# Performance work log

Measured on AMD Instinct MI355X. Metric: run time of the kernel, lower is better.

Reference implementation:

```python
import jax, jax.numpy as jnp
import numpy as np

SCALING = 16.0 / 16  # lora_alpha / rank
INIT_THRESHOLD = 0.01


def setup_inputs() -> dict:
    key = jax.random.key(0)
    k1, k2, k3, k4, k5 = jax.random.split(key, 5)
    B, S, D, R = 4, 2048, 4096, 16
    x = jax.random.normal(k1, (B, S, D), dtype=jnp.float32)
    weight = jax.random.normal(k2, (D, D), dtype=jnp.float32) * (1.0 / np.sqrt(D))
    lora_A = jax.random.normal(k3, (R, D), dtype=jnp.float32) * 0.01
    lora_B = jax.random.normal(k4, (D, R), dtype=jnp.float32) * 0.02
    lora_sigma = jax.random.normal(k5, (R,), dtype=jnp.float32)
    return {"x": x, "weight": weight, "lora_A": lora_A, "lora_B": lora_B,
            "lora_sigma": lora_sigma}


def reference(x, weight, lora_A, lora_B, lora_sigma):
    # mask out singular values below threshold, scale B columns
    mask = (jnp.abs(lora_sigma) >= INIT_THRESHOLD).astype(lora_sigma.dtype)
    sigma_masked = lora_sigma * mask                     # [R]
    # delta = (B * sigma) @ A, scaled; materialized as in original module
    delta = (lora_B * sigma_masked[None, :]) @ lora_A    # [out, in]
    delta = delta * SCALING
    base_out = jnp.einsum('bsd,od->bso', x, weight)      # F.linear(x, W)
    lora_out = jnp.einsum('bsd,od->bso', x, delta)       # dropout p=0 -> identity
    return base_out + lora_out
```

## Files before the change

### kernel.cpp

```cpp
#include <hip/hip_runtime.h>

#define D_DIM 4096
#define R_DIM 16
#define SCALING_F 1.0f
#define THRESH 0.01f

typedef __attribute__((ext_vector_type(8))) short short8;
typedef __attribute__((ext_vector_type(4))) float floatx4;

__device__ __forceinline__ unsigned int f2bf(float f) {
  union { float f; unsigned int u; } v; v.f = f;
  unsigned int u = v.u;
  u += 0x7FFFu + ((u >> 16) & 1u);
  return u >> 16;
}

__global__ __launch_bounds__(256) void convert_x_kernel(
    const float* __restrict__ x, unsigned int* __restrict__ xb, int n8) {
  int idx = blockIdx.x * 256 + threadIdx.x;
  if (idx >= n8) return;
  const float4* xp = (const float4*)x;
  float4 v0 = xp[2 * idx];
  float4 v1 = xp[2 * idx + 1];
  uint4 o;
  o.x = f2bf(v0.x) | (f2bf(v0.y) << 16);
  o.y = f2bf(v0.z) | (f2bf(v0.w) << 16);
  o.z = f2bf(v1.x) | (f2bf(v1.y) << 16);
  o.w = f2bf(v1.z) | (f2bf(v1.w) << 16);
  ((uint4*)xb)[idx] = o;
}

__global__ __launch_bounds__(256) void build_weff_kernel(
    const float* __restrict__ W, const float* __restrict__ lA,
    const float* __restrict__ lB, const float* __restrict__ sigma,
    unsigned int* __restrict__ wb) {
  __shared__ float Bs[R_DIM];
  int idx = blockIdx.x * 256 + threadIdx.x;
  int o  = idx >> 10;
  int dq = idx & 1023;
  if (threadIdx.x < R_DIM) {
    float s = sigma[threadIdx.x];
    s = (fabsf(s) >= THRESH) ? s : 0.0f;
    Bs[threadIdx.x] = lB[o * R_DIM + threadIdx.x] * s * SCALING_F;
  }
  __syncthreads();
  float4 acc = ((const float4*)W)[idx];
#pragma unroll
  for (int r = 0; r < R_DIM; ++r) {
    float b = Bs[r];
    float4 a = ((const float4*)(lA + (size_t)r * D_DIM))[dq];
    acc.x += b * a.x; acc.y += b * a.y; acc.z += b * a.z; acc.w += b * a.w;
  }
  uint2 p;
  p.x = f2bf(acc.x) | (f2bf(acc.y) << 16);
  p.y = f2bf(acc.z) | (f2bf(acc.w) << 16);
  ((uint2*)wb)[idx] = p;
}


__device__ __forceinline__ void stage16(const void* g, void* l) {
  __builtin_amdgcn_global_load_lds(
      (const __attribute__((address_space(1))) void*)g,
      (__attribute__((address_space(3))) void*)l, 16, 0, 0);
}

#define LOADA(BUF, QM)                                                         \
  _Pragma("unroll") for (int t = 0; t < 4; ++t) {                              \
    af[t][0] = *(const short8*)(aRd0 + (BUF)*32768 + (QM)*16384 + t*2048);     \
    af[t][1] = *(const short8*)(aRd1 + (BUF)*32768 + (QM)*16384 + t*2048);     \
  }

#define LOADB(BUF, QN)                                                         \
  _Pragma("unroll") for (int j = 0; j < 2; ++j) {                              \
    bf[j][0] = *(const short8*)(bRd0 + (BUF)*32768 + (QN)*16384 + j*2048);     \
    bf[j][1] = *(const short8*)(bRd1 + (BUF)*32768 + (QN)*16384 + j*2048);     \
  }

#define MFMAQ(QM, QN)                                                          \
  _Pragma("unroll") for (int t = 0; t < 4; ++t)                                \
  _Pragma("unroll") for (int j = 0; j < 2; ++j)                                \
    acc[QM][QN][t][j] = __builtin_amdgcn_mfma_f32_16x16x32_bf16(               \
        af[t][0], bf[j][0], acc[QM][QN][t][j], 0, 0, 0);                       \
  _Pragma("unroll") for (int t = 0; t < 4; ++t)                                \
  _Pragma("unroll") for (int j = 0; j < 2; ++j)                                \
    acc[QM][QN][t][j] = __builtin_amdgcn_mfma_f32_16x16x32_bf16(               \
        af[t][1], bf[j][1], acc[QM][QN][t][j], 0, 0, 0);

#define SYNC_MID()                                      \
  __builtin_amdgcn_sched_barrier(0);                    \
  __builtin_amdgcn_s_barrier();                         \
  asm volatile("s_waitcnt lgkmcnt(0)" ::: "memory");    \
  __builtin_amdgcn_sched_barrier(0);                    \
  __builtin_amdgcn_s_setprio(1)

#define SYNC_END()                                      \
  __builtin_amdgcn_s_setprio(0);                        \
  __builtin_amdgcn_sched_barrier(0);                    \
  __builtin_amdgcn_s_barrier();                         \
  __builtin_amdgcn_sched_barrier(0)

#define SYNC_END_VM()                                   \
  __builtin_amdgcn_s_setprio(0);                        \
  __builtin_amdgcn_sched_barrier(0);                    \
  asm volatile("s_waitcnt vmcnt(4)" ::: "memory");      \
  __builtin_amdgcn_s_barrier();                         \
  __builtin_amdgcn_sched_barrier(0)

__global__ __launch_bounds__(512, 2) void gemm_bt_kernel(
    const unsigned short* __restrict__ A,
    const unsigned short* __restrict__ B,
    float* __restrict__ C, int M) {
  __shared__ __align__(16) char lds[131072];

  const int tid  = threadIdx.x;
  const int lane = tid & 63;
  const int wave = tid >> 6;
  const int wm   = wave >> 2;
  const int wn   = wave & 3;
  const int lrow = lane & 15;
  const int lq   = lane >> 4;
  const int r7   = lrow & 7;

  const int bid = blockIdx.x;
  const int cpx = gridDim.x >> 3;
  const int swz = (bid & 7) * cpx + (bid >> 3);
  const int m0 = (swz >> 4) << 8;
  const int n0 = (swz & 15) << 8;

  const int rr8  = tid >> 3;
  const int kgsw = (tid & 7) ^ (rr8 & 7);
  const char* aSrc = (const char*)A + ((size_t)(m0 + rr8) << 13) + (kgsw << 4);
  const int nrow = (rr8 & 31) | ((rr8 & 32) << 1);
  const char* bSrc = (const char*)B + ((size_t)(n0 + nrow) << 13) + (kgsw << 4);
  char* ldsW = lds + wave * 1024;

  const char* aRd0 = lds + wm * 8192 + lrow * 128 + ((lq ^ r7) << 4);
  const char* aRd1 = lds + wm * 8192 + lrow * 128 + (((4 | lq) ^ r7) << 4);
  const char* bRd0 = lds + 65536 + wn * 4096 + lrow * 128 + ((lq ^ r7) << 4);
  const char* bRd1 = lds + 65536 + wn * 4096 + lrow * 128 + (((4 | lq) ^ r7) << 4);

  short8 af[4][2], bf[2][2];
  floatx4 acc[2][2][4][2] = {};

  stage16(aSrc,                     ldsW + 0);
  stage16(aSrc + (128 << 13),       ldsW + 8192);
  stage16(aSrc + (64 << 13),        ldsW + 16384);
  stage16(aSrc + (192 << 13),       ldsW + 24576);
  stage16(bSrc,                     ldsW + 65536);
  stage16(bSrc + (128 << 13),       ldsW + 73728);
  stage16(bSrc + (32 << 13),        ldsW + 81920);
  stage16(bSrc + (160 << 13),       ldsW + 90112);
  stage16(aSrc + 128,               ldsW + 32768);
  stage16(aSrc + (128 << 13) + 128, ldsW + 40960);
  stage16(bSrc + (32 << 13) + 128,  ldsW + 114688);
  stage16(bSrc + (160 << 13) + 128, ldsW + 122880);
  asm volatile("s_waitcnt vmcnt(4)" ::: "memory");
  __builtin_amdgcn_s_barrier();
  __builtin_amdgcn_sched_barrier(0);

  int kb = 0;
#pragma unroll 1
  for (int f = 0; f < 32; ++f) {
    const int k1 = (kb + 128) & 8191;
    const int k2 = (kb + 256) & 8191;
    const int k3 = (kb + 384) & 8191;

    LOADA(0, 0) LOADB(0, 0)
    stage16(aSrc + (64 << 13) + k1,  ldsW + 49152);
    stage16(aSrc + (192 << 13) + k1, ldsW + 57344);
    SYNC_MID();
    MFMAQ(0, 0)
    SYNC_END();

    LOADB(0, 1)
    stage16(bSrc + k1,               ldsW + 98304);
    stage16(bSrc + (128 << 13) + k1, ldsW + 106496);
    SYNC_MID();
    MFMAQ(0, 1)
    SYNC_END();

    LOADA(0, 1)
    stage16(aSrc + k2,               ldsW + 0);
    stage16(aSrc + (128 << 13) + k2, ldsW + 8192);
    SYNC_MID();
    MFMAQ(1, 1)
    SYNC_END();

    LOADB(0, 0)
    stage16(bSrc + (32 << 13) + k2,  ldsW + 81920);
    stage16(bSrc + (160 << 13) + k2, ldsW + 90112);
    SYNC_MID();
    MFMAQ(1, 0)
    SYNC_END_VM();

    LOADA(1, 0) LOADB(1, 0)
    stage16(aSrc + (64 << 13) + k2,  ldsW + 16384);
    stage16(aSrc + (192 << 13) + k2, ldsW + 24576);
    SYNC_MID();
    MFMAQ(0, 0)
    SYNC_END();

    LOADB(1, 1)
    stage16(bSrc + k2,               ldsW + 65536);
    stage16(bSrc + (128 << 13) + k2, ldsW + 73728);
    SYNC_MID();
    MFMAQ(0, 1)
    SYNC_END();

    LOADA(1, 1)
    stage16(aSrc + k3,               ldsW + 32768);
    stage16(aSrc + (128 << 13) + k3, ldsW + 40960);
    SYNC_MID();
    MFMAQ(1, 1)
    SYNC_END();

    LOADB(1, 0)
    stage16(bSrc + (32 << 13) + k3,  ldsW + 114688);
    stage16(bSrc + (160 << 13) + k3, ldsW + 122880);
    SYNC_MID();
    MFMAQ(1, 0)
    SYNC_END_VM();

    kb += 256;
  }

#pragma unroll
  for (int qm = 0; qm < 2; ++qm)
#pragma unroll
    for (int t = 0; t < 4; ++t)
#pragma unroll
      for (int rr = 0; rr < 4; ++rr) {
        float* cp = C +
            (size_t)(m0 + wm * 128 + qm * 64 + t * 16 + lq * 4 + rr) * D_DIM +
            n0 + wn * 64 + lrow;
#pragma unroll
        for (int qn = 0; qn < 2; ++qn)
#pragma unroll
          for (int j = 0; j < 2; ++j)
            cp[qn * 32 + j * 16] = acc[qm][qn][t][j][rr];
      }
}

extern "C" void kernel_launch(void* const* d_in, const int* in_sizes, int n_in,
                              void* d_out, int out_size, void* d_ws, size_t ws_size,
                              hipStream_t stream) {
  const float* x     = (const float*)d_in[0];
  const float* W     = (const float*)d_in[1];
  const float* lA    = (const float*)d_in[2];
  const float* lB    = (const float*)d_in[3];
  const float* sigma = (const float*)d_in[4];
  float* out = (float*)d_out;

  const int M = in_sizes[0] / D_DIM;
  unsigned int* xb = (unsigned int*)d_ws;
  unsigned int* wb = (unsigned int*)((char*)d_ws + (size_t)M * D_DIM * 2);

  const int n8 = in_sizes[0] / 8;
  convert_x_kernel<<<(n8 + 255) / 256, 256, 0, stream>>>(x, xb, n8);

  const int wquads = (D_DIM * D_DIM) / 4;
  build_weff_kernel<<<wquads / 256, 256, 0, stream>>>(W, lA, lB, sigma, wb);

  const int nblocks = (M / 256) * (D_DIM / 256);
  gemm_bt_kernel<<<nblocks, 512, 0, stream>>>(
      (const unsigned short*)xb, (const unsigned short*)wb, out, M);
}
```

Measured before the change: 524.5 us.

## Software-pipeline LDS fragment loads across MFMA phases and merge prep kernels

Restructures the GEMM main loop so LDS-to-register fragment loads for the next phase are issued before the current phase's MFMAs. It uses double-buffered A/B register fragments and partial lgkmcnt waits, with one barrier per phase in place of two. The staging order and vmcnt depth change to keep eight global-to-LDS loads in flight. Separately, the x-conversion and weight-build kernels are fused into a single launch. The aim is to hide LDS latency and barrier overhead, at the cost of more registers and more delicate hazard ordering across the shared LDS buffers.

```diff
diff --git a/kernel.cpp b/kernel.cpp
--- a/kernel.cpp
+++ b/kernel.cpp
@@ -15,46 +15,48 @@
   return u >> 16;
 }
 
-__global__ __launch_bounds__(256) void convert_x_kernel(
-    const float* __restrict__ x, unsigned int* __restrict__ xb, int n8) {
-  int idx = blockIdx.x * 256 + threadIdx.x;
-  if (idx >= n8) return;
-  const float4* xp = (const float4*)x;
-  float4 v0 = xp[2 * idx];
-  float4 v1 = xp[2 * idx + 1];
-  uint4 o;
-  o.x = f2bf(v0.x) | (f2bf(v0.y) << 16);
-  o.y = f2bf(v0.z) | (f2bf(v0.w) << 16);
-  o.z = f2bf(v1.x) | (f2bf(v1.y) << 16);
-  o.w = f2bf(v1.z) | (f2bf(v1.w) << 16);
-  ((uint4*)xb)[idx] = o;
-}
-
-__global__ __launch_bounds__(256) void build_weff_kernel(
+__global__ __launch_bounds__(256) void prep_kernel(
+    const float* __restrict__ x, unsigned int* __restrict__ xb, int n8,
+    int nxblocks,
     const float* __restrict__ W, const float* __restrict__ lA,
     const float* __restrict__ lB, const float* __restrict__ sigma,
     unsigned int* __restrict__ wb) {
   __shared__ float Bs[R_DIM];
-  int idx = blockIdx.x * 256 + threadIdx.x;
-  int o  = idx >> 10;
-  int dq = idx & 1023;
-  if (threadIdx.x < R_DIM) {
-    float s = sigma[threadIdx.x];
-    s = (fabsf(s) >= THRESH) ? s : 0.0f;
-    Bs[threadIdx.x] = lB[o * R_DIM + threadIdx.x] * s * SCALING_F;
-  }
-  __syncthreads();
-  float4 acc = ((const float4*)W)[idx];
-#pragma unroll
-  for (int r = 0; r < R_DIM; ++r) {
-    float b = Bs[r];
-    float4 a = ((const float4*)(lA + (size_t)r * D_DIM))[dq];
-    acc.x += b * a.x; acc.y += b * a.y; acc.z += b * a.z; acc.w += b * a.w;
-  }
-  uint2 p;
-  p.x = f2bf(acc.x) | (f2bf(acc.y) << 16);
-  p.y = f2bf(acc.z) | (f2bf(acc.w) << 16);
-  ((uint2*)wb)[idx] = p;
+  int b = blockIdx.x;
+  if (b < nxblocks) {
+    int idx = b * 256 + threadIdx.x;
+    if (idx >= n8) return;
+    const float4* xp = (const float4*)x;
+    float4 v0 = xp[2 * idx];
+    float4 v1 = xp[2 * idx + 1];
+    uint4 o;
+    o.x = f2bf(v0.x) | (f2bf(v0.y) << 16);
+    o.y = f2bf(v0.z) | (f2bf(v0.w) << 16);
+    o.z = f2bf(v1.x) | (f2bf(v1.y) << 16);
+    o.w = f2bf(v1.z) | (f2bf(v1.w) << 16);
+    ((uint4*)xb)[idx] = o;
+  } else {
+    int idx = (b - nxblocks) * 256 + threadIdx.x;
+    int o  = idx >> 10;
+    int dq = idx & 1023;
+    if (threadIdx.x < R_DIM) {
+      float s = sigma[threadIdx.x];
+      s = (fabsf(s) >= THRESH) ? s : 0.0f;
+      Bs[threadIdx.x] = lB[o * R_DIM + threadIdx.x] * s * SCALING_F;
+    }
+    __syncthreads();
+    float4 acc = ((const float4*)W)[idx];
+#pragma unroll
+    for (int r = 0; r < R_DIM; ++r) {
+      float bb = Bs[r];
+      float4 a = ((const float4*)(lA + (size_t)r * D_DIM))[dq];
+      acc.x += bb * a.x; acc.y += bb * a.y; acc.z += bb * a.z; acc.w += bb * a.w;
+    }
+    uint2 p;
+    p.x = f2bf(acc.x) | (f2bf(acc.y) << 16);
+    p.y = f2bf(acc.z) | (f2bf(acc.w) << 16);
+    ((uint2*)wb)[idx] = p;
+  }
 }
 
 
@@ -64,47 +66,42 @@
       (__attribute__((address_space(3))) void*)l, 16, 0, 0);
 }
 
-#define LOADA(BUF, QM)                                                         \
+#define FENCE() __builtin_amdgcn_sched_barrier(0)
+
+#define WAIT_VM8_BAR()                                  \
+  FENCE();                                              \
+  asm volatile("s_waitcnt vmcnt(8)" ::: "memory");      \
+  __builtin_amdgcn_s_barrier();                         \
+  FENCE()
+
+#define WAIT_LGKM(N)                                    \
+  asm volatile("s_waitcnt lgkmcnt(" #N ")" ::: "memory"); \
+  FENCE()
+
+#define LOADA_TO(DST, BUF, QM)                                                 \
   _Pragma("unroll") for (int t = 0; t < 4; ++t) {                              \
-    af[t][0] = *(const short8*)(aRd0 + (BUF)*32768 + (QM)*16384 + t*2048);     \
-    af[t][1] = *(const short8*)(aRd1 + (BUF)*32768 + (QM)*16384 + t*2048);     \
-  }
-
-#define LOADB(BUF, QN)                                                         \
+    DST[t][0] = *(const short8*)(aRd0 + (BUF)*32768 + (QM)*16384 + t*2048);    \
+    DST[t][1] = *(const short8*)(aRd1 + (BUF)*32768 + (QM)*16384 + t*2048);    \
+  }
+
+#define LOADB_TO(DST, BUF, QN)                                                 \
   _Pragma("unroll") for (int j = 0; j < 2; ++j) {                              \
-    bf[j][0] = *(const short8*)(bRd0 + (BUF)*32768 + (QN)*16384 + j*2048);     \
-    bf[j][1] = *(const short8*)(bRd1 + (BUF)*32768 + (QN)*16384 + j*2048);     \
-  }
-
-#define MFMAQ(QM, QN)                                                          \
+    DST[j][0] = *(const short8*)(bRd0 + (BUF)*32768 + (QN)*16384 + j*2048);    \
+    DST[j][1] = *(const short8*)(bRd1 + (BUF)*32768 + (QN)*16384 + j*2048);    \
+  }
+
+#define MFMA16(QM, QN, AF, BF)                                                 \
+  __builtin_amdgcn_s_setprio(1);                                               \
   _Pragma("unroll") for (int t = 0; t < 4; ++t)                                \
   _Pragma("unroll") for (int j = 0; j < 2; ++j)                                \
     acc[QM][QN][t][j] = __builtin_amdgcn_mfma_f32_16x16x32_bf16(               \
-        af[t][0], bf[j][0], acc[QM][QN][t][j], 0, 0, 0);                       \
+        AF[t][0], BF[j][0], acc[QM][QN][t][j], 0, 0, 0);                       \
   _Pragma("unroll") for (int t = 0; t < 4; ++t)                                \
   _Pragma("unroll") for (int j = 0; j < 2; ++j)                                \
     acc[QM][QN][t][j] = __builtin_amdgcn_mfma_f32_16x16x32_bf16(               \
-        af[t][1], bf[j][1], acc[QM][QN][t][j], 0, 0, 0);
-
-#define SYNC_MID()                                      \
-  __builtin_amdgcn_sched_barrier(0);                    \
-  __builtin_amdgcn_s_barrier();                         \
-  asm volatile("s_waitcnt lgkmcnt(0)" ::: "memory");    \
-  __builtin_amdgcn_sched_barrier(0);                    \
-  __builtin_amdgcn_s_setprio(1)
-
-#define SYNC_END()                                      \
-  __builtin_amdgcn_s_setprio(0);                        \
-  __builtin_amdgcn_sched_barrier(0);                    \
-  __builtin_amdgcn_s_barrier();                         \
-  __builtin_amdgcn_sched_barrier(0)
-
-#define SYNC_END_VM()                                   \
-  __builtin_amdgcn_s_setprio(0);                        \
-  __builtin_amdgcn_sched_barrier(0);                    \
-  asm volatile("s_waitcnt vmcnt(4)" ::: "memory");      \
-  __builtin_amdgcn_s_barrier();                         \
-  __builtin_amdgcn_sched_barrier(0)
+        AF[t][1], BF[j][1], acc[QM][QN][t][j], 0, 0, 0);                       \
+  __builtin_amdgcn_s_setprio(0);                                               \
+  FENCE()
 
 __global__ __launch_bounds__(512, 2) void gemm_bt_kernel(
     const unsigned short* __restrict__ A,
@@ -139,24 +136,30 @@
   const char* bRd0 = lds + 65536 + wn * 4096 + lrow * 128 + ((lq ^ r7) << 4);
   const char* bRd1 = lds + 65536 + wn * 4096 + lrow * 128 + (((4 | lq) ^ r7) << 4);
 
-  short8 af[4][2], bf[2][2];
+  short8 afX[4][2], afY[4][2];
+  short8 bf0A[2][2], bf0B[2][2];
+  short8 bf1[2][2];
   floatx4 acc[2][2][4][2] = {};
 
-  stage16(aSrc,                     ldsW + 0);
-  stage16(aSrc + (128 << 13),       ldsW + 8192);
-  stage16(aSrc + (64 << 13),        ldsW + 16384);
-  stage16(aSrc + (192 << 13),       ldsW + 24576);
-  stage16(bSrc,                     ldsW + 65536);
-  stage16(bSrc + (128 << 13),       ldsW + 73728);
-  stage16(bSrc + (32 << 13),        ldsW + 81920);
-  stage16(bSrc + (160 << 13),       ldsW + 90112);
-  stage16(aSrc + 128,               ldsW + 32768);
-  stage16(aSrc + (128 << 13) + 128, ldsW + 40960);
-  stage16(bSrc + (32 << 13) + 128,  ldsW + 114688);
-  stage16(bSrc + (160 << 13) + 128, ldsW + 122880);
-  asm volatile("s_waitcnt vmcnt(4)" ::: "memory");
+  stage16(aSrc,                      ldsW + 0);
+  stage16(aSrc + (128 << 13),        ldsW + 8192);
+  stage16(bSrc,                      ldsW + 65536);
+  stage16(bSrc + (128 << 13),        ldsW + 73728);
+  stage16(bSrc + (32 << 13),         ldsW + 81920);
+  stage16(bSrc + (160 << 13),        ldsW + 90112);
+  stage16(aSrc + (64 << 13),         ldsW + 16384);
+  stage16(aSrc + (192 << 13),        ldsW + 24576);
+  stage16(aSrc + 128,                ldsW + 32768);
+  stage16(aSrc + (128 << 13) + 128,  ldsW + 40960);
+  stage16(bSrc + 128,                ldsW + 98304);
+  stage16(bSrc + (128 << 13) + 128,  ldsW + 106496);
+  FENCE();
+  asm volatile("s_waitcnt vmcnt(8)" ::: "memory");
   __builtin_amdgcn_s_barrier();
-  __builtin_amdgcn_sched_barrier(0);
+  FENCE();
+  LOADA_TO(afX, 0, 0)
+  LOADB_TO(bf0A, 0, 0)
+  FENCE();
 
   int kb = 0;
 #pragma unroll 1
@@ -165,61 +168,61 @@
     const int k2 = (kb + 256) & 8191;
     const int k3 = (kb + 384) & 8191;
 
-    LOADA(0, 0) LOADB(0, 0)
+    stage16(bSrc + (32 << 13) + k1,  ldsW + 114688);
+    stage16(bSrc + (160 << 13) + k1, ldsW + 122880);
+    WAIT_VM8_BAR();
+    LOADB_TO(bf1, 0, 1)
+    WAIT_LGKM(4);
+    MFMA16(0, 0, afX, bf0A);
+
     stage16(aSrc + (64 << 13) + k1,  ldsW + 49152);
     stage16(aSrc + (192 << 13) + k1, ldsW + 57344);
-    SYNC_MID();
-    MFMAQ(0, 0)
-    SYNC_END();
-
-    LOADB(0, 1)
-    stage16(bSrc + k1,               ldsW + 98304);
-    stage16(bSrc + (128 << 13) + k1, ldsW + 106496);
-    SYNC_MID();
-    MFMAQ(0, 1)
-    SYNC_END();
-
-    LOADA(0, 1)
+    WAIT_VM8_BAR();
+    LOADA_TO(afY, 0, 1)
+    WAIT_LGKM(8);
+    MFMA16(0, 1, afX, bf1);
+
     stage16(aSrc + k2,               ldsW + 0);
     stage16(aSrc + (128 << 13) + k2, ldsW + 8192);
-    SYNC_MID();
-    MFMAQ(1, 1)
-    SYNC_END();
-
-    LOADB(0, 0)
+    WAIT_VM8_BAR();
+    LOADA_TO(afX, 1, 0)
+    WAIT_LGKM(8);
+    MFMA16(1, 1, afY, bf1);
+
+    stage16(bSrc + k2,               ldsW + 65536);
+    stage16(bSrc + (128 << 13) + k2, ldsW + 73728);
+    WAIT_VM8_BAR();
+    LOADB_TO(bf0B, 1, 0)
+    WAIT_LGKM(4);
+    MFMA16(1, 0, afY, bf0A);
+
     stage16(bSrc + (32 << 13) + k2,  ldsW + 81920);
     stage16(bSrc + (160 << 13) + k2, ldsW + 90112);
-    SYNC_MID();
-    MFMAQ(1, 0)
-    SYNC_END_VM();
-
-    LOADA(1, 0) LOADB(1, 0)
+    WAIT_VM8_BAR();
+    LOADB_TO(bf1, 1, 1)
+    WAIT_LGKM(4);
+    MFMA16(0, 0, afX, bf0B);
+
     stage16(aSrc + (64 << 13) + k2,  ldsW + 16384);
     stage16(aSrc + (192 << 13) + k2, ldsW + 24576);
-    SYNC_MID();
-    MFMAQ(0, 0)
-    SYNC_END();
-
-    LOADB(1, 1)
-    stage16(bSrc + k2,               ldsW + 65536);
-    stage16(bSrc + (128 << 13) + k2, ldsW + 73728);
-    SYNC_MID();
-    MFMAQ(0, 1)
-    SYNC_END();
-
-    LOADA(1, 1)
+    WAIT_VM8_BAR();
+    LOADA_TO(afY, 1, 1)
+    WAIT_LGKM(8);
+    MFMA16(0, 1, afX, bf1);
+
     stage16(aSrc + k3,               ldsW + 32768);
     stage16(aSrc + (128 << 13) + k3, ldsW + 40960);
-    SYNC_MID();
-    MFMAQ(1, 1)
-    SYNC_END();
-
-    LOADB(1, 0)
-    stage16(bSrc + (32 << 13) + k3,  ldsW + 114688);
-    stage16(bSrc + (160 << 13) + k3, ldsW + 122880);
-    SYNC_MID();
-    MFMAQ(1, 0)
-    SYNC_END_VM();
+    WAIT_VM8_BAR();
+    LOADA_TO(afX, 0, 0)
+    WAIT_LGKM(8);
+    MFMA16(1, 1, afY, bf1);
+
+    stage16(bSrc + k3,               ldsW + 98304);
+    stage16(bSrc + (128 << 13) + k3, ldsW + 106496);
+    WAIT_VM8_BAR();
+    LOADB_TO(bf0A, 0, 0)
+    WAIT_LGKM(4);
+    MFMA16(1, 0, afY, bf0B);
 
     kb += 256;
   }
@@ -256,10 +259,10 @@
   unsigned int* wb = (unsigned int*)((char*)d_ws + (size_t)M * D_DIM * 2);
 
   const int n8 = in_sizes[0] / 8;
-  convert_x_kernel<<<(n8 + 255) / 256, 256, 0, stream>>>(x, xb, n8);
-
-  const int wquads = (D_DIM * D_DIM) / 4;
-  build_weff_kernel<<<wquads / 256, 256, 0, stream>>>(W, lA, lB, sigma, wb);
+  const int nxblocks = (n8 + 255) / 256;
+  const int nwblocks = (D_DIM * D_DIM / 4) / 256;
+  prep_kernel<<<nxblocks + nwblocks, 256, 0, stream>>>(
+      x, xb, n8, nxblocks, W, lA, lB, sigma, wb);
 
   const int nblocks = (M / 256) * (D_DIM / 256);
   gemm_bt_kernel<<<nblocks, 512, 0, stream>>>(
```

After: 524.5 us. Within noise of the previous version (+0.0%).

## Switch GEMM to 32x32x16 MFMA and merge prep kernels into one launch

Applied to the files above, without the earlier changes.

The GEMM inner loop moves from 16x16x32 bf16 MFMA tiles to 32x32x16 tiles. This changes the LDS fragment read pattern, the accumulator layout and the epilogue store mapping, and should cut LDS reads per FLOP and the number of MFMA instructions issued. The x conversion and effective-weight build kernels are fused into one launch that branches on block index, which removes one kernel launch. The risks are extra register pressure from the larger 16-float accumulators and possible LDS bank conflicts from the new swizzled read addresses.

```diff
diff --git a/kernel.cpp b/kernel.cpp
--- a/kernel.cpp
+++ b/kernel.cpp
@@ -6,7 +6,7 @@
 #define THRESH 0.01f
 
 typedef __attribute__((ext_vector_type(8))) short short8;
-typedef __attribute__((ext_vector_type(4))) float floatx4;
+typedef __attribute__((ext_vector_type(16))) float floatx16;
 
 __device__ __forceinline__ unsigned int f2bf(float f) {
   union { float f; unsigned int u; } v; v.f = f;
@@ -15,46 +15,48 @@
   return u >> 16;
 }
 
-__global__ __launch_bounds__(256) void convert_x_kernel(
-    const float* __restrict__ x, unsigned int* __restrict__ xb, int n8) {
-  int idx = blockIdx.x * 256 + threadIdx.x;
-  if (idx >= n8) return;
-  const float4* xp = (const float4*)x;
-  float4 v0 = xp[2 * idx];
-  float4 v1 = xp[2 * idx + 1];
-  uint4 o;
-  o.x = f2bf(v0.x) | (f2bf(v0.y) << 16);
-  o.y = f2bf(v0.z) | (f2bf(v0.w) << 16);
-  o.z = f2bf(v1.x) | (f2bf(v1.y) << 16);
-  o.w = f2bf(v1.z) | (f2bf(v1.w) << 16);
-  ((uint4*)xb)[idx] = o;
-}
-
-__global__ __launch_bounds__(256) void build_weff_kernel(
+__global__ __launch_bounds__(256) void prep_kernel(
+    const float* __restrict__ x, unsigned int* __restrict__ xb, int n8,
+    int nxblocks,
     const float* __restrict__ W, const float* __restrict__ lA,
     const float* __restrict__ lB, const float* __restrict__ sigma,
     unsigned int* __restrict__ wb) {
   __shared__ float Bs[R_DIM];
-  int idx = blockIdx.x * 256 + threadIdx.x;
-  int o  = idx >> 10;
-  int dq = idx & 1023;
-  if (threadIdx.x < R_DIM) {
-    float s = sigma[threadIdx.x];
-    s = (fabsf(s) >= THRESH) ? s : 0.0f;
-    Bs[threadIdx.x] = lB[o * R_DIM + threadIdx.x] * s * SCALING_F;
+  int b = blockIdx.x;
+  if (b < nxblocks) {
+    int idx = b * 256 + threadIdx.x;
+    if (idx >= n8) return;
+    const float4* xp = (const float4*)x;
+    float4 v0 = xp[2 * idx];
+    float4 v1 = xp[2 * idx + 1];
+    uint4 o;
+    o.x = f2bf(v0.x) | (f2bf(v0.y) << 16);
+    o.y = f2bf(v0.z) | (f2bf(v0.w) << 16);
+    o.z = f2bf(v1.x) | (f2bf(v1.y) << 16);
+    o.w = f2bf(v1.z) | (f2bf(v1.w) << 16);
+    ((uint4*)xb)[idx] = o;
+  } else {
+    int idx = (b - nxblocks) * 256 + threadIdx.x;
+    int o  = idx >> 10;
+    int dq = idx & 1023;
+    if (threadIdx.x < R_DIM) {
+      float s = sigma[threadIdx.x];
+      s = (fabsf(s) >= THRESH) ? s : 0.0f;
+      Bs[threadIdx.x] = lB[o * R_DIM + threadIdx.x] * s * SCALING_F;
+    }
+    __syncthreads();
+    float4 acc = ((const float4*)W)[idx];
+#pragma unroll
+    for (int r = 0; r < R_DIM; ++r) {
+      float bb = Bs[r];
+      float4 a = ((const float4*)(lA + (size_t)r * D_DIM))[dq];
+      acc.x += bb * a.x; acc.y += bb * a.y; acc.z += bb * a.z; acc.w += bb * a.w;
+    }
+    uint2 p;
+    p.x = f2bf(acc.x) | (f2bf(acc.y) << 16);
+    p.y = f2bf(acc.z) | (f2bf(acc.w) << 16);
+    ((uint2*)wb)[idx] = p;
   }
-  __syncthreads();
-  float4 acc = ((const float4*)W)[idx];
-#pragma unroll
-  for (int r = 0; r < R_DIM; ++r) {
-    float b = Bs[r];
-    float4 a = ((const float4*)(lA + (size_t)r * D_DIM))[dq];
-    acc.x += b * a.x; acc.y += b * a.y; acc.z += b * a.z; acc.w += b * a.w;
-  }
-  uint2 p;
-  p.x = f2bf(acc.x) | (f2bf(acc.y) << 16);
-  p.y = f2bf(acc.z) | (f2bf(acc.w) << 16);
-  ((uint2*)wb)[idx] = p;
 }
 
 
@@ -64,47 +66,48 @@
       (__attribute__((address_space(3))) void*)l, 16, 0, 0);
 }
 
-#define LOADA(BUF, QM)                                                         \
-  _Pragma("unroll") for (int t = 0; t < 4; ++t) {                              \
-    af[t][0] = *(const short8*)(aRd0 + (BUF)*32768 + (QM)*16384 + t*2048);     \
-    af[t][1] = *(const short8*)(aRd1 + (BUF)*32768 + (QM)*16384 + t*2048);     \
-  }
-
-#define LOADB(BUF, QN)                                                         \
-  _Pragma("unroll") for (int j = 0; j < 2; ++j) {                              \
-    bf[j][0] = *(const short8*)(bRd0 + (BUF)*32768 + (QN)*16384 + j*2048);     \
-    bf[j][1] = *(const short8*)(bRd1 + (BUF)*32768 + (QN)*16384 + j*2048);     \
-  }
-
-#define MFMAQ(QM, QN)                                                          \
-  _Pragma("unroll") for (int t = 0; t < 4; ++t)                                \
-  _Pragma("unroll") for (int j = 0; j < 2; ++j)                                \
-    acc[QM][QN][t][j] = __builtin_amdgcn_mfma_f32_16x16x32_bf16(               \
-        af[t][0], bf[j][0], acc[QM][QN][t][j], 0, 0, 0);                       \
-  _Pragma("unroll") for (int t = 0; t < 4; ++t)                                \
-  _Pragma("unroll") for (int j = 0; j < 2; ++j)                                \
-    acc[QM][QN][t][j] = __builtin_amdgcn_mfma_f32_16x16x32_bf16(               \
-        af[t][1], bf[j][1], acc[QM][QN][t][j], 0, 0, 0);
+#define FENCE() __builtin_amdgcn_sched_barrier(0)
 
 #define SYNC_MID()                                      \
-  __builtin_amdgcn_sched_barrier(0);                    \
+  FENCE();                                              \
   __builtin_amdgcn_s_barrier();                         \
   asm volatile("s_waitcnt lgkmcnt(0)" ::: "memory");    \
-  __builtin_amdgcn_sched_barrier(0);                    \
-  __builtin_amdgcn_s_setprio(1)
+  FENCE()
 
 #define SYNC_END()                                      \
-  __builtin_amdgcn_s_setprio(0);                        \
-  __builtin_amdgcn_sched_barrier(0);                    \
+  FENCE();                                              \
   __builtin_amdgcn_s_barrier();                         \
-  __builtin_amdgcn_sched_barrier(0)
+  FENCE()
 
 #define SYNC_END_VM()                                   \
-  __builtin_amdgcn_s_setprio(0);                        \
-  __builtin_amdgcn_sched_barrier(0);                    \
+  FENCE();                                              \
   asm volatile("s_waitcnt vmcnt(4)" ::: "memory");      \
   __builtin_amdgcn_s_barrier();                         \
-  __builtin_amdgcn_sched_barrier(0)
+  FENCE()
+
+#define LOADA32(BUF, QM)                                                       \
+  _Pragma("unroll") for (int s = 0; s < 4; ++s) {                              \
+    aF[0][s] = *(const short8*)(aRdB + (BUF)*32768 + (QM)*16384 +              \
+                                (((2*s + kh) ^ r7) << 4));                     \
+    aF[1][s] = *(const short8*)(aRdB + (BUF)*32768 + (QM)*16384 + 4096 +       \
+                                (((2*s + kh) ^ r7) << 4));                     \
+  }
+
+#define LOADB32(BUF, QN)                                                       \
+  _Pragma("unroll") for (int s = 0; s < 4; ++s)                                \
+    bF[s] = *(const short8*)(bRdB + (BUF)*32768 + (QN)*16384 +                 \
+                             (((2*s + kh) ^ r7) << 4));
+
+#define MFMAQ32(QM, QN)                                                        \
+  __builtin_amdgcn_s_setprio(1);                                               \
+  _Pragma("unroll") for (int s = 0; s < 4; ++s) {                              \
+    acc[QM][QN][0] = __builtin_amdgcn_mfma_f32_32x32x16_bf16(                  \
+        aF[0][s], bF[s], acc[QM][QN][0], 0, 0, 0);                             \
+    acc[QM][QN][1] = __builtin_amdgcn_mfma_f32_32x32x16_bf16(                  \
+        aF[1][s], bF[s], acc[QM][QN][1], 0, 0, 0);                             \
+  }                                                                            \
+  __builtin_amdgcn_s_setprio(0);                                               \
+  FENCE()
 
 __global__ __launch_bounds__(512, 2) void gemm_bt_kernel(
     const unsigned short* __restrict__ A,
@@ -117,9 +120,9 @@
   const int wave = tid >> 6;
   const int wm   = wave >> 2;
   const int wn   = wave & 3;
-  const int lrow = lane & 15;
-  const int lq   = lane >> 4;
-  const int r7   = lrow & 7;
+  const int l31  = lane & 31;
+  const int kh   = lane >> 5;
+  const int r7   = l31 & 7;
 
   const int bid = blockIdx.x;
   const int cpx = gridDim.x >> 3;
@@ -134,13 +137,11 @@
   const char* bSrc = (const char*)B + ((size_t)(n0 + nrow) << 13) + (kgsw << 4);
   char* ldsW = lds + wave * 1024;
 
-  const char* aRd0 = lds + wm * 8192 + lrow * 128 + ((lq ^ r7) << 4);
-  const char* aRd1 = lds + wm * 8192 + lrow * 128 + (((4 | lq) ^ r7) << 4);
-  const char* bRd0 = lds + 65536 + wn * 4096 + lrow * 128 + ((lq ^ r7) << 4);
-  const char* bRd1 = lds + 65536 + wn * 4096 + lrow * 128 + (((4 | lq) ^ r7) << 4);
-
-  short8 af[4][2], bf[2][2];
-  floatx4 acc[2][2][4][2] = {};
+  const char* aRdB = lds + wm * 8192 + l31 * 128;
+  const char* bRdB = lds + 65536 + wn * 4096 + l31 * 128;
+
+  short8 aF[2][4], bF[4];
+  floatx16 acc[2][2][2] = {};
 
   stage16(aSrc,                     ldsW + 0);
   stage16(aSrc + (128 << 13),       ldsW + 8192);
@@ -154,9 +155,10 @@
   stage16(aSrc + (128 << 13) + 128, ldsW + 40960);
   stage16(bSrc + (32 << 13) + 128,  ldsW + 114688);
   stage16(bSrc + (160 << 13) + 128, ldsW + 122880);
+  FENCE();
   asm volatile("s_waitcnt vmcnt(4)" ::: "memory");
   __builtin_amdgcn_s_barrier();
-  __builtin_amdgcn_sched_barrier(0);
+  FENCE();
 
   int kb = 0;
 #pragma unroll 1
@@ -165,60 +167,60 @@
     const int k2 = (kb + 256) & 8191;
     const int k3 = (kb + 384) & 8191;
 
-    LOADA(0, 0) LOADB(0, 0)
+    LOADA32(0, 0) LOADB32(0, 0)
     stage16(aSrc + (64 << 13) + k1,  ldsW + 49152);
     stage16(aSrc + (192 << 13) + k1, ldsW + 57344);
     SYNC_MID();
-    MFMAQ(0, 0)
-    SYNC_END();
-
-    LOADB(0, 1)
+    MFMAQ32(0, 0);
+    SYNC_END();
+
+    LOADB32(0, 1)
     stage16(bSrc + k1,               ldsW + 98304);
     stage16(bSrc + (128 << 13) + k1, ldsW + 106496);
     SYNC_MID();
-    MFMAQ(0, 1)
-    SYNC_END();
-
-    LOADA(0, 1)
+    MFMAQ32(0, 1);
+    SYNC_END();
+
+    LOADA32(0, 1)
     stage16(aSrc + k2,               ldsW + 0);
     stage16(aSrc + (128 << 13) + k2, ldsW + 8192);
     SYNC_MID();
-    MFMAQ(1, 1)
-    SYNC_END();
-
-    LOADB(0, 0)
+    MFMAQ32(1, 1);
+    SYNC_END();
+
+    LOADB32(0, 0)
     stage16(bSrc + (32 << 13) + k2,  ldsW + 81920);
     stage16(bSrc + (160 << 13) + k2, ldsW + 90112);
     SYNC_MID();
-    MFMAQ(1, 0)
+    MFMAQ32(1, 0);
     SYNC_END_VM();
 
-    LOADA(1, 0) LOADB(1, 0)
+    LOADA32(1, 0) LOADB32(1, 0)
     stage16(aSrc + (64 << 13) + k2,  ldsW + 16384);
     stage16(aSrc + (192 << 13) + k2, ldsW + 24576);
     SYNC_MID();
-    MFMAQ(0, 0)
-    SYNC_END();
-
-    LOADB(1, 1)
+    MFMAQ32(0, 0);
+    SYNC_END();
+
+    LOADB32(1, 1)
     stage16(bSrc + k2,               ldsW + 65536);
     stage16(bSrc + (128 << 13) + k2, ldsW + 73728);
     SYNC_MID();
-    MFMAQ(0, 1)
-    SYNC_END();
-
-    LOADA(1, 1)
+    MFMAQ32(0, 1);
+    SYNC_END();
+
+    LOADA32(1, 1)
     stage16(aSrc + k3,               ldsW + 32768);
     stage16(aSrc + (128 << 13) + k3, ldsW + 40960);
     SYNC_MID();
-    MFMAQ(1, 1)
-    SYNC_END();
-
-    LOADB(1, 0)
+    MFMAQ32(1, 1);
+    SYNC_END();
+
+    LOADB32(1, 0)
     stage16(bSrc + (32 << 13) + k3,  ldsW + 114688);
     stage16(bSrc + (160 << 13) + k3, ldsW + 122880);
     SYNC_MID();
-    MFMAQ(1, 0)
+    MFMAQ32(1, 0);
     SYNC_END_VM();
 
     kb += 256;
@@ -227,18 +229,17 @@
 #pragma unroll
   for (int qm = 0; qm < 2; ++qm)
 #pragma unroll
-    for (int t = 0; t < 4; ++t)
-#pragma unroll
-      for (int rr = 0; rr < 4; ++rr) {
-        float* cp = C +
-            (size_t)(m0 + wm * 128 + qm * 64 + t * 16 + lq * 4 + rr) * D_DIM +
-            n0 + wn * 64 + lrow;
-#pragma unroll
-        for (int qn = 0; qn < 2; ++qn)
-#pragma unroll
-          for (int j = 0; j < 2; ++j)
-            cp[qn * 32 + j * 16] = acc[qm][qn][t][j][rr];
-      }
+    for (int i2 = 0; i2 < 2; ++i2)
+#pragma unroll
+      for (int g = 0; g < 4; ++g)
+#pragma unroll
+        for (int rr = 0; rr < 4; ++rr) {
+          const int row = m0 + wm * 128 + qm * 64 + i2 * 32 +
+                          g * 8 + kh * 4 + rr;
+          float* cp = C + (size_t)row * D_DIM + n0 + wn * 64 + l31;
+          cp[0]  = acc[qm][0][i2][g * 4 + rr];
+          cp[32] = acc[qm][1][i2][g * 4 + rr];
+        }
 }
 
 extern "C" void kernel_launch(void* const* d_in, const int* in_sizes, int n_in,
@@ -256,10 +257,10 @@
   unsigned int* wb = (unsigned int*)((char*)d_ws + (size_t)M * D_DIM * 2);
 
   const int n8 = in_sizes[0] / 8;
-  convert_x_kernel<<<(n8 + 255) / 256, 256, 0, stream>>>(x, xb, n8);
-
-  const int wquads = (D_DIM * D_DIM) / 4;
-  build_weff_kernel<<<wquads / 256, 256, 0, stream>>>(W, lA, lB, sigma, wb);
+  const int nxblocks = (n8 + 255) / 256;
+  const int nwblocks = (D_DIM * D_DIM / 4) / 256;
+  prep_kernel<<<nxblocks + nwblocks, 256, 0, stream>>>(
+      x, xb, n8, nxblocks, W, lA, lB, sigma, wb);
 
   const int nblocks = (M / 256) * (D_DIM / 256);
   gemm_bt_kernel<<<nblocks, 512, 0, stream>>>(
```

New measurement: 552.5 us. 5.3% more time.
